# Performance work log

Measured on AMD Instinct MI355X. Metric: run time of the kernel, lower is better.

The kernel has to match this reference:

```python
import jax, jax.numpy as jnp
import numpy as np

NUM_HEADS = 4
SP = 2  # split_size


def haar_dwt(x):
    # Orthonormal Haar (db1) single-level DWT on even-sized [B,C,H,W].
    a = x[:, :, 0::2, 0::2]
    b = x[:, :, 0::2, 1::2]
    c = x[:, :, 1::2, 0::2]
    d = x[:, :, 1::2, 1::2]
    ll = (a + b + c + d) * 0.5
    lh = (-a - b + c + d) * 0.5  # vertical detail
    hl = (-a + b - c + d) * 0.5  # horizontal detail
    hh = (a - b - c + d) * 0.5   # diagonal detail
    return ll, lh, hl, hh


def haar_idwt(ll, lh, hl, hh):
    a = (ll - lh - hl + hh) * 0.5
    b = (ll - lh + hl - hh) * 0.5
    c = (ll + lh - hl - hh) * 0.5
    d = (ll + lh + hl + hh) * 0.5
    B, C, H2, W2 = ll.shape
    top = jnp.stack([a, b], axis=-1)          # [B,C,H2,W2,2]
    bot = jnp.stack([c, d], axis=-1)          # [B,C,H2,W2,2]
    y = jnp.stack([top, bot], axis=3)          # [B,C,H2,2,W2,2]
    return y.reshape(B, C, 2 * H2, 2 * W2)


def conv1x1(w, x):
    # w: [out_c, in_c]; x: [B,in_c,H,W]
    return jnp.einsum('oc,bchw->bohw', w, x)


def window_attn(q, k, v, scale):
    # Channel attention within non-overlapping SPxSP windows.
    # rearrange 'b (c head) (h hsp) (w wsp) -> (b h w) head c (hsp wsp)'
    B, CH, H, W = q.shape
    c = CH // NUM_HEADS
    h, w = H // SP, W // SP

    def to_win(t):
        t = t.reshape(B, c, NUM_HEADS, h, SP, w, SP)
        t = t.transpose(0, 3, 5, 2, 1, 4, 6)   # B,h,w,head,c,SPh,SPw
        return t.reshape(B, h, w, NUM_HEADS, c, SP * SP)

    qw = to_win(q) * scale
    kw = to_win(k)
    vw = to_win(v)
    attn = jax.nn.softmax(jnp.einsum('bhwncs,bhwnds->bhwncd', qw, kw), axis=-1)
    out = jnp.einsum('bhwncd,bhwnds->bhwncs', attn, vw)
    out = out.reshape(B, h, w, NUM_HEADS, c, SP, SP)
    out = out.transpose(0, 4, 3, 1, 5, 2, 6)   # B,c,head,h,SPh,w,SPw
    return out.reshape(B, CH, H, W)


def setup_inputs() -> dict:
    key = jax.random.key(0)
    k1, k2, k3 = jax.random.split(key, 3)
    dim = 64
    x = jax.random.normal(k1, (8, dim, 256, 256), dtype=jnp.float32)
    w_qkv_lh = jax.random.normal(k2, (3 * dim, dim), dtype=jnp.float32) * 0.05
    w_qkv_m = jax.random.normal(k3, (3 * 2 * dim, 2 * dim), dtype=jnp.float32) * 0.05
    return {"x": x, "w_qkv_lh": w_qkv_lh, "w_qkv_m": w_qkv_m}


def reference(x, w_qkv_lh, w_qkv_m):
    ll, lh, hl, hh = haar_dwt(x)
    low = ll
    mid = jnp.concatenate([lh, hl], axis=1)   # [B,2C,H/2,W/2]
    high = hh
    C = low.shape[1]
    lh_scale = float((C // NUM_HEADS) ** -0.5)
    m_scale = float((2 * C // NUM_HEADS) ** -0.5)

    lq, lk, lv = jnp.split(conv1x1(w_qkv_lh, low), 3, axis=1)
    mq, mk, mv = jnp.split(conv1x1(w_qkv_m, mid), 3, axis=1)
    hq, hk, hv = jnp.split(conv1x1(w_qkv_lh, high), 3, axis=1)

    x_low = window_attn(lq, lk, lv, lh_scale)
    x_mid = window_attn(mq, mk, mv, m_scale)
    x_high = window_attn(hq, hk, hv, lh_scale)

    lh2, hl2 = jnp.split(x_mid, 2, axis=1)
    return haar_idwt(x_low, lh2, hl2, x_high)
```

## Files before the change

### kernel.cpp

```cpp
#include <hip/hip_runtime.h>
#include <stdint.h>


typedef _Float16 halfT;
typedef __attribute__((ext_vector_type(2))) _Float16 half2T;
typedef __attribute__((ext_vector_type(8))) _Float16 half8;
typedef __attribute__((ext_vector_type(4))) float f32x4;

union H8 { half8 v; half2T h2[4]; uint16_t s[8]; };
union H2U { half2T h; uint32_t u; };

static __device__ __forceinline__ uint16_t f2h(float f){
  union { halfT h; uint16_t u; } x; x.h = (halfT)f; return x.u;
}
static __device__ __forceinline__ float h2f(uint16_t u){
  union { uint16_t u; halfT h; } x; x.u = u; return (float)x.h;
}
static __device__ __forceinline__ float dot4(half2T a0, half2T a1,
                                             half2T b0, half2T b1){
#if __has_builtin(__builtin_amdgcn_fdot2)
  return __builtin_amdgcn_fdot2(a1, b1, __builtin_amdgcn_fdot2(a0, b0, 0.f, false), false);
#else
  half2T p = a0*b0 + a1*b1;
  return (float)p.x + (float)p.y;
#endif
}
static __device__ __forceinline__ half2T pk2(float e){
#if __has_builtin(__builtin_amdgcn_cvt_pkrtz)
  union { __fp16 __attribute__((ext_vector_type(2))) p; half2T h; } c;
  c.p = __builtin_amdgcn_cvt_pkrtz(e, e);
  return c.h;
#else
  half2T r; r.x = (halfT)e; r.y = (halfT)e; return r;
#endif
}

__global__ void k_wt(const float* __restrict__ wlh, const float* __restrict__ wm,
                     halfT* __restrict__ wH){
  int i = blockIdx.x * 256 + threadIdx.x;
  if (i < 12288)      wH[i] = (halfT)wlh[i];
  else if (i < 61440) wH[i] = (halfT)wm[i - 12288];
}

#define OT_CS 276
#define OT_RS 68

static __device__ __forceinline__ int qidx(int G, int np, int W){
  return G*256 + np*128 + ((W ^ (G & 7)) << 3);
}

static __device__ __forceinline__ void conv64(const halfT* __restrict__ w,
    const uint16_t* __restrict__ bands, uint16_t* __restrict__ qk,
    int band, int mrow, int g, int ms, int pxb, int wl, int qq){
  half8 bfr[2];
  #pragma unroll
  for (int ks = 0; ks < 2; ++ks){
    H8 t; int cb = ks*32 + g*8;
    #pragma unroll
    for (int k = 0; k < 8; ++k)
      t.s[k] = bands[band*4096 + (cb + k)*64 + (pxb ^ (g << 4))];
    bfr[ks] = t.v;
  }
  #pragma unroll
  for (int mi = 0; mi < 6; ++mi){
    int mt = ms*6 + mi;
    f32x4 acc = {0.f,0.f,0.f,0.f};
    #pragma unroll
    for (int ks = 0; ks < 2; ++ks){
      half8 a = *(const half8*)&w[(mt*16 + mrow)*64 + ks*32 + g*8];
      acc = __builtin_amdgcn_mfma_f32_16x16x32_f16(a, bfr[ks], acc, 0, 0, 0);
    }
    #pragma unroll
    for (int r = 0; r < 4; ++r){
      int tl = mt*16 + g*4 + r;
      qk[qidx(tl >> 2, (tl & 3) >> 1, wl) + (tl & 1)*4 + qq] = f2h(acc[r]);
    }
  }
}

static __device__ __forceinline__ void attn16p(const uint16_t* __restrict__ qk,
    int m, int np, int W, uint32_t* __restrict__ yslab, int tid){
  const halfT sh = (halfT)0.25f;
  const half8 s8 = {sh,sh,sh,sh,sh,sh,sh,sh};
  H8 qg; qg.v = (*(const half8*)&qk[qidx(m >> 1, np, W)]) * s8;
  float sum0 = 0.f, sum1 = 0.f;
  half2T A0 = {(halfT)0,(halfT)0}, A1 = A0, B0 = A0, B1 = A0;
  #pragma unroll
  for (int d = 0; d < 16; ++d){
    H8 kg, vg;
    kg.v = *(const half8*)&qk[qidx(16 + d, np, W)];
    vg.v = *(const half8*)&qk[qidx(32 + d, np, W)];
    float a0 = dot4(qg.h2[0], qg.h2[1], kg.h2[0], kg.h2[1]);
    float a1 = dot4(qg.h2[2], qg.h2[3], kg.h2[2], kg.h2[3]);
    float e0 = __expf(a0), e1 = __expf(a1);
    sum0 += e0; sum1 += e1;
    half2T p0 = pk2(e0), p1 = pk2(e1);
    A0 += p0*vg.h2[0]; A1 += p0*vg.h2[1];
    B0 += p1*vg.h2[2]; B1 += p1*vg.h2[3];
  }
  halfT i0 = (halfT)__builtin_amdgcn_rcpf(sum0);
  halfT i1 = (halfT)__builtin_amdgcn_rcpf(sum1);
  half2T v0 = {i0,i0}, v1 = {i1,i1};
  H2U u0, u1, u2, u3;
  u0.h = A0*v0; u1.h = A1*v0; u2.h = B0*v1; u3.h = B1*v1;
  yslab[0*512 + tid] = u0.u;
  yslab[1*512 + tid] = u1.u;
  yslab[2*512 + tid] = u2.u;
  yslab[3*512 + tid] = u3.u;
}

#define IDWT(CH, Y0, Y1, Y2, Y3) { \
  float* otc = ot + (CH)*OT_CS + gw*4; \
  _Pragma("unroll") \
  for (int rp = 0; rp < 2; ++rp){ \
    float4 top, bot; \
    _Pragma("unroll") \
    for (int cp = 0; cp < 2; ++cp){ \
      int s2 = rp*2 + cp; \
      float ll = Y0[s2], lh = Y1[s2], hl = Y2[s2], hh = Y3[s2]; \
      float va = 0.5f*(ll - lh - hl + hh); \
      float vb = 0.5f*(ll - lh + hl - hh); \
      float vc = 0.5f*(ll + lh - hl - hh); \
      float vd = 0.5f*(ll + lh + hl + hh); \
      if (cp == 0){ top.x = va; top.y = vb; bot.x = vc; bot.y = vd; } \
      else        { top.z = va; top.w = vb; bot.z = vc; bot.w = vd; } \
    } \
    *(float4*)&otc[(2*rp)*OT_RS]   = top; \
    *(float4*)&otc[(2*rp+1)*OT_RS] = bot; \
  } }

__global__ __launch_bounds__(512, 4) void k_fused(const float* __restrict__ x,
    const halfT* __restrict__ wH, float* __restrict__ out){
  __shared__ __align__(16) uint8_t smem[81920];
  uint16_t* bands = (uint16_t*)smem;
  uint16_t* qk    = (uint16_t*)(smem + 32768);
  uint32_t* ybuf  = (uint32_t*)smem;
  float*    ot    = (float*)smem;

  const int tid = threadIdx.x;
  const int wv = tid >> 6, lane = tid & 63;
  const int unit = blockIdx.x >> 2, q4 = blockIdx.x & 3;
  const int b = unit >> 6, hw = unit & 63;
  const int col0 = q4 * 64;
  const float* xb = x + (size_t)b * 64 * 65536;
  const halfT* wM = wH + 12288;

  #pragma unroll
  for (int it = 0; it < 4; ++it){
    int idx = it*512 + tid;
    int j = idx & 15, rp = (idx >> 4) & 1, c = idx >> 5;
    const float* src = xb + (size_t)c*65536 + (size_t)(4*hw + 2*rp)*256 + col0 + 4*j;
    float4 r0 = *(const float4*)src;
    float4 r1 = *(const float4*)(src + 256);
    float v0[4], v1[4];
    v0[0] = 0.5f*( r0.x + r0.y + r1.x + r1.y);
    v0[1] = 0.5f*(-r0.x - r0.y + r1.x + r1.y);
    v0[2] = 0.5f*(-r0.x + r0.y - r1.x + r1.y);
    v0[3] = 0.5f*( r0.x - r0.y - r1.x + r1.y);
    v1[0] = 0.5f*( r0.z + r0.w + r1.z + r1.w);
    v1[1] = 0.5f*(-r0.z - r0.w + r1.z + r1.w);
    v1[2] = 0.5f*(-r0.z + r0.w - r1.z + r1.w);
    v1[3] = 0.5f*( r0.z - r0.w - r1.z + r1.w);
    int base = c*64 + ((rp*32 + 2*j) ^ (((c >> 3) & 3) << 4));
    #pragma unroll
    for (int bb = 0; bb < 4; ++bb)
      *(uint32_t*)&bands[bb*4096 + base] =
          (uint32_t)f2h(v0[bb]) | ((uint32_t)f2h(v1[bb]) << 16);
  }
  __syncthreads();

  const int mrow = lane & 15, g = lane >> 4;
  const int m = lane & 31;
  const int W = wv*2 + (lane >> 5);
  const int A = 2*m;
  const int np = m & 1;
  const int pxb = (wv & 3)*16 + mrow;
  const int wl = (pxb & 31) >> 1, qq = (pxb >> 5)*2 + (pxb & 1);
  const int ms = wv >> 2;

  conv64(wH, bands, qk, 0, mrow, g, ms, pxb, wl, qq);
  __syncthreads();
  attn16p(qk, m, np, W, ybuf + 0*2048, tid);
  __syncthreads();

  {
    half8 bfr[4];
    #pragma unroll
    for (int ks = 0; ks < 4; ++ks){
      H8 t; int band = 1 + (ks >> 1); int cb = (ks & 1)*32 + g*8;
      #pragma unroll
      for (int k = 0; k < 8; ++k)
        t.s[k] = bands[band*4096 + (cb + k)*64 + (pxb ^ (g << 4))];
      bfr[ks] = t.v;
    }
    #pragma unroll
    for (int mi = 0; mi < 12; ++mi){
      int mt = ms*12 + mi;
      f32x4 acc = {0.f,0.f,0.f,0.f};
      #pragma unroll
      for (int ks = 0; ks < 4; ++ks){
        half8 a = *(const half8*)&wM[(mt*16 + mrow)*128 + ks*32 + g*8];
        acc = __builtin_amdgcn_mfma_f32_16x16x32_f16(a, bfr[ks], acc, 0, 0, 0);
      }
      #pragma unroll
      for (int r = 0; r < 4; ++r){
        int tl = mt*16 + g*4 + r;
        qk[qidx(tl >> 2, (tl & 3) >> 1, wl) + (tl & 1)*4 + qq] = f2h(acc[r]);
      }
    }
  }
  __syncthreads();

  {
    const halfT shm = (halfT)0.17677669529663687f;
    const half8 s8m = {shm,shm,shm,shm,shm,shm,shm,shm};
    H8 qa, qb;
    qa.v = (*(const half8*)&qk[qidx(m >> 1, np, W)]) * s8m;
    qb.v = (*(const half8*)&qk[qidx(16 + (m >> 1), np, W)]) * s8m;
    float sm0 = 0.f, sm1 = 0.f, sm2 = 0.f, sm3 = 0.f;
    half2T P0a = {(halfT)0,(halfT)0}, P0b = P0a, P1a = P0a, P1b = P0a;
    half2T P2a = P0a, P2b = P0a, P3a = P0a, P3b = P0a;
    #pragma unroll
    for (int dl = 0; dl < 32; ++dl){
      H8 kg, vg;
      kg.v = *(const half8*)&qk[qidx(32 + dl, np, W)];
      vg.v = *(const half8*)&qk[qidx(64 + dl, np, W)];
      float a0 = dot4(qa.h2[0], qa.h2[1], kg.h2[0], kg.h2[1]);
      float a1 = dot4(qa.h2[2], qa.h2[3], kg.h2[2], kg.h2[3]);
      float a2 = dot4(qb.h2[0], qb.h2[1], kg.h2[0], kg.h2[1]);
      float a3 = dot4(qb.h2[2], qb.h2[3], kg.h2[2], kg.h2[3]);
      float e0 = __expf(a0), e1 = __expf(a1);
      float e2 = __expf(a2), e3 = __expf(a3);
      sm0 += e0; sm1 += e1; sm2 += e2; sm3 += e3;
      half2T p0 = pk2(e0), p1 = pk2(e1), p2 = pk2(e2), p3 = pk2(e3);
      P0a += p0*vg.h2[0]; P0b += p0*vg.h2[1];
      P1a += p1*vg.h2[2]; P1b += p1*vg.h2[3];
      P2a += p2*vg.h2[0]; P2b += p2*vg.h2[1];
      P3a += p3*vg.h2[2]; P3b += p3*vg.h2[3];
    }
    halfT i0 = (halfT)__builtin_amdgcn_rcpf(sm0);
    halfT i1 = (halfT)__builtin_amdgcn_rcpf(sm1);
    halfT i2 = (halfT)__builtin_amdgcn_rcpf(sm2);
    halfT i3 = (halfT)__builtin_amdgcn_rcpf(sm3);
    half2T v0 = {i0,i0}, v1 = {i1,i1}, v2 = {i2,i2}, v3 = {i3,i3};
    uint32_t* y1s = ybuf + 1*2048;
    uint32_t* y2s = ybuf + 2*2048;
    H2U a0u, a1u, b0u, b1u, c0u, c1u, d0u, d1u;
    a0u.h = P0a*v0; a1u.h = P0b*v0; b0u.h = P1a*v1; b1u.h = P1b*v1;
    c0u.h = P2a*v2; c1u.h = P2b*v2; d0u.h = P3a*v3; d1u.h = P3b*v3;
    y1s[0*512 + tid] = a0u.u;
    y1s[1*512 + tid] = a1u.u;
    y1s[2*512 + tid] = b0u.u;
    y1s[3*512 + tid] = b1u.u;
    y2s[0*512 + tid] = c0u.u;
    y2s[1*512 + tid] = c1u.u;
    y2s[2*512 + tid] = d0u.u;
    y2s[3*512 + tid] = d1u.u;
  }
  __syncthreads();

  conv64(wH, bands, qk, 3, mrow, g, ms, pxb, wl, qq);
  __syncthreads();
  attn16p(qk, m, np, W, ybuf + 3*2048, tid);

  float ya[4][2][4];
  #pragma unroll
  for (int p = 0; p < 4; ++p){
    #pragma unroll
    for (int w = 0; w < 4; ++w){
      uint32_t u = ybuf[p*2048 + w*512 + tid];
      ya[p][w >> 1][(w & 1)*2 + 0] = h2f((uint16_t)(u & 0xffffu));
      ya[p][w >> 1][(w & 1)*2 + 1] = h2f((uint16_t)(u >> 16));
    }
  }
  __syncthreads();

  {
    const int gw = W ^ (m & 15);
    IDWT(A,     ya[0][0], ya[1][0], ya[2][0], ya[3][0]);
    IDWT(A + 1, ya[0][1], ya[1][1], ya[2][1], ya[3][1]);
  }
  __syncthreads();

  #pragma unroll
  for (int it = 0; it < 2; ++it){
    int s = it*512 + tid;
    int ch = s >> 4, row = (s >> 2) & 3, seg = s & 3;
    int sw = (ch >> 1) & 15;
    const float* rowp = &ot[ch*OT_CS + row*OT_RS];
    float4 v0 = *(const float4*)&rowp[((seg*4+0) ^ sw)*4];
    float4 v1 = *(const float4*)&rowp[((seg*4+1) ^ sw)*4];
    float4 v2 = *(const float4*)&rowp[((seg*4+2) ^ sw)*4];
    float4 v3 = *(const float4*)&rowp[((seg*4+3) ^ sw)*4];
    float* dst = out + (((size_t)b*64 + ch)*256 + (size_t)(4*hw + row))*256 + col0 + seg*16;
    ((float4*)dst)[0] = v0; ((float4*)dst)[1] = v1;
    ((float4*)dst)[2] = v2; ((float4*)dst)[3] = v3;
  }
}

extern "C" void kernel_launch(void* const* d_in, const int* in_sizes, int n_in,
                              void* d_out, int out_size, void* d_ws, size_t ws_size,
                              hipStream_t stream){
  const float* x   = (const float*)d_in[0];
  const float* wlh = (const float*)d_in[1];
  const float* wm  = (const float*)d_in[2];
  float* out = (float*)d_out;
  halfT* wH = (halfT*)d_ws;

  hipLaunchKernelGGL(k_wt,    dim3(240),  dim3(256), 0, stream, wlh, wm, wH);
  hipLaunchKernelGGL(k_fused, dim3(2048), dim3(512), 0, stream, x, wH, out);
}
```

Baseline: 204.1 us.

## Double-buffer qk for low/high bands and chunk attention loops to cut barriers

The high-band 1x1 conv now writes into a second qk buffer (offset QKB) right after the low-band attention, with no barrier between them, so one __syncthreads pair is removed and the two band stages can overlap. The attention loops over d are also restructured from full unroll into rolled outer chunks of four, with all K/V loads of a chunk issued before the compute. This lowers code size and register pressure but relies on the shared qk allocation being large enough for two buffers. It also changes instruction scheduling, with some risk of exposed LDS latency.

Measured after the change: 217.6 us. 6.6% more time.

```diff
diff --git a/kernel.cpp b/kernel.cpp
--- a/kernel.cpp
+++ b/kernel.cpp
@@ -44,6 +44,7 @@
 
 #define OT_CS 276
 #define OT_RS 68
+#define QKB   12288
 
 static __device__ __forceinline__ int qidx(int G, int np, int W){
   return G*256 + np*128 + ((W ^ (G & 7)) << 3);
@@ -85,18 +86,23 @@
   H8 qg; qg.v = (*(const half8*)&qk[qidx(m >> 1, np, W)]) * s8;
   float sum0 = 0.f, sum1 = 0.f;
   half2T A0 = {(halfT)0,(halfT)0}, A1 = A0, B0 = A0, B1 = A0;
-  #pragma unroll
-  for (int d = 0; d < 16; ++d){
-    H8 kg, vg;
-    kg.v = *(const half8*)&qk[qidx(16 + d, np, W)];
-    vg.v = *(const half8*)&qk[qidx(32 + d, np, W)];
-    float a0 = dot4(qg.h2[0], qg.h2[1], kg.h2[0], kg.h2[1]);
-    float a1 = dot4(qg.h2[2], qg.h2[3], kg.h2[2], kg.h2[3]);
-    float e0 = __expf(a0), e1 = __expf(a1);
-    sum0 += e0; sum1 += e1;
-    half2T p0 = pk2(e0), p1 = pk2(e1);
-    A0 += p0*vg.h2[0]; A1 += p0*vg.h2[1];
-    B0 += p1*vg.h2[2]; B1 += p1*vg.h2[3];
+  for (int dc = 0; dc < 4; ++dc){
+    H8 kg[4], vg[4];
+    #pragma unroll
+    for (int t = 0; t < 4; ++t){
+      kg[t].v = *(const half8*)&qk[qidx(16 + dc*4 + t, np, W)];
+      vg[t].v = *(const half8*)&qk[qidx(32 + dc*4 + t, np, W)];
+    }
+    #pragma unroll
+    for (int t = 0; t < 4; ++t){
+      float a0 = dot4(qg.h2[0], qg.h2[1], kg[t].h2[0], kg[t].h2[1]);
+      float a1 = dot4(qg.h2[2], qg.h2[3], kg[t].h2[2], kg[t].h2[3]);
+      float e0 = __expf(a0), e1 = __expf(a1);
+      sum0 += e0; sum1 += e1;
+      half2T p0 = pk2(e0), p1 = pk2(e1);
+      A0 += p0*vg[t].h2[0]; A1 += p0*vg[t].h2[1];
+      B0 += p1*vg[t].h2[2]; B1 += p1*vg[t].h2[3];
+    }
   }
   halfT i0 = (halfT)__builtin_amdgcn_rcpf(sum0);
   halfT i1 = (halfT)__builtin_amdgcn_rcpf(sum1);
@@ -180,7 +186,12 @@
 
   conv64(wH, bands, qk, 0, mrow, g, ms, pxb, wl, qq);
   __syncthreads();
+
   attn16p(qk, m, np, W, ybuf + 0*2048, tid);
+  conv64(wH, bands, qk + QKB, 3, mrow, g, ms, pxb, wl, qq);
+  __syncthreads();
+
+  attn16p(qk + QKB, m, np, W, ybuf + 3*2048, tid);
   __syncthreads();
 
   {
@@ -220,23 +231,28 @@
     float sm0 = 0.f, sm1 = 0.f, sm2 = 0.f, sm3 = 0.f;
     half2T P0a = {(halfT)0,(halfT)0}, P0b = P0a, P1a = P0a, P1b = P0a;
     half2T P2a = P0a, P2b = P0a, P3a = P0a, P3b = P0a;
-    #pragma unroll
-    for (int dl = 0; dl < 32; ++dl){
-      H8 kg, vg;
-      kg.v = *(const half8*)&qk[qidx(32 + dl, np, W)];
-      vg.v = *(const half8*)&qk[qidx(64 + dl, np, W)];
-      float a0 = dot4(qa.h2[0], qa.h2[1], kg.h2[0], kg.h2[1]);
-      float a1 = dot4(qa.h2[2], qa.h2[3], kg.h2[2], kg.h2[3]);
-      float a2 = dot4(qb.h2[0], qb.h2[1], kg.h2[0], kg.h2[1]);
-      float a3 = dot4(qb.h2[2], qb.h2[3], kg.h2[2], kg.h2[3]);
-      float e0 = __expf(a0), e1 = __expf(a1);
-      float e2 = __expf(a2), e3 = __expf(a3);
-      sm0 += e0; sm1 += e1; sm2 += e2; sm3 += e3;
-      half2T p0 = pk2(e0), p1 = pk2(e1), p2 = pk2(e2), p3 = pk2(e3);
-      P0a += p0*vg.h2[0]; P0b += p0*vg.h2[1];
-      P1a += p1*vg.h2[2]; P1b += p1*vg.h2[3];
-      P2a += p2*vg.h2[0]; P2b += p2*vg.h2[1];
-      P3a += p3*vg.h2[2]; P3b += p3*vg.h2[3];
+    for (int dc = 0; dc < 8; ++dc){
+      H8 kg[4], vg[4];
+      #pragma unroll
+      for (int t = 0; t < 4; ++t){
+        kg[t].v = *(const half8*)&qk[qidx(32 + dc*4 + t, np, W)];
+        vg[t].v = *(const half8*)&qk[qidx(64 + dc*4 + t, np, W)];
+      }
+      #pragma unroll
+      for (int t = 0; t < 4; ++t){
+        float a0 = dot4(qa.h2[0], qa.h2[1], kg[t].h2[0], kg[t].h2[1]);
+        float a1 = dot4(qa.h2[2], qa.h2[3], kg[t].h2[2], kg[t].h2[3]);
+        float a2 = dot4(qb.h2[0], qb.h2[1], kg[t].h2[0], kg[t].h2[1]);
+        float a3 = dot4(qb.h2[2], qb.h2[3], kg[t].h2[2], kg[t].h2[3]);
+        float e0 = __expf(a0), e1 = __expf(a1);
+        float e2 = __expf(a2), e3 = __expf(a3);
+        sm0 += e0; sm1 += e1; sm2 += e2; sm3 += e3;
+        half2T p0 = pk2(e0), p1 = pk2(e1), p2 = pk2(e2), p3 = pk2(e3);
+        P0a += p0*vg[t].h2[0]; P0b += p0*vg[t].h2[1];
+        P1a += p1*vg[t].h2[2]; P1b += p1*vg[t].h2[3];
+        P2a += p2*vg[t].h2[0]; P2b += p2*vg[t].h2[1];
+        P3a += p3*vg[t].h2[2]; P3b += p3*vg[t].h2[3];
+      }
     }
     halfT i0 = (halfT)__builtin_amdgcn_rcpf(sm0);
     halfT i1 = (halfT)__builtin_amdgcn_rcpf(sm1);
@@ -257,11 +273,6 @@
     y2s[2*512 + tid] = d0u.u;
     y2s[3*512 + tid] = d1u.u;
   }
-  __syncthreads();
-
-  conv64(wH, bands, qk, 3, mrow, g, ms, pxb, wl, qq);
-  __syncthreads();
-  attn16p(qk, m, np, W, ybuf + 3*2048, tid);
 
   float ya[4][2][4];
   #pragma unroll
```
